# Optimization experiments

Measured on AMD Instinct MI355X. Metric: run time of the kernel, lower is better.

The kernel has to match this reference:

```python
import jax, jax.numpy as jnp
import numpy as np

N, E, IN, H, C = 50000, 400000, 128, 8, 32
NEG_SLOPE = 0.2


def setup_inputs() -> dict:
    key = jax.random.key(0)
    ks = jax.random.split(key, 8)
    s = 0.1
    return {
        "x": jax.random.normal(ks[0], (N, IN), jnp.float32),
        "edge_index": jax.random.randint(ks[1], (2, E), 0, N, dtype=jnp.int32),
        "edge_attr": jax.random.normal(ks[2], (E, 1), jnp.float32),
        "batch": jnp.zeros((N,), jnp.int32),
        "W_l": jax.random.normal(ks[3], (H * C, IN), jnp.float32) * s,
        "W_r": jax.random.normal(ks[4], (H * C, IN), jnp.float32) * s,
        "W_e": jax.random.normal(ks[5], (H * C, 1), jnp.float32) * s,
        "att": jax.random.normal(ks[6], (H, C), jnp.float32) * s,
        "bias": jnp.zeros((C,), jnp.float32),
        "W_proj": jax.random.normal(ks[7], (C, IN), jnp.float32) * s,
    }


def reference(x, edge_index, edge_attr, batch, W_l, W_r, W_e, att, bias, W_proj):
    n = x.shape[0]
    # --- add self loops (PyG default), edge_attr fill = 'mean' ---
    loop = jnp.arange(n, dtype=edge_index.dtype)
    ei = jnp.concatenate([edge_index, jnp.stack([loop, loop])], axis=1)  # [2, E+N]
    loop_attr = jnp.broadcast_to(edge_attr.mean(axis=0), (n, edge_attr.shape[1]))
    ea = jnp.concatenate([edge_attr, loop_attr], axis=0)                 # [E+N, 1]
    src, dst = ei[0], ei[1]

    # --- node transforms (GATv2: separate lin_l / lin_r) ---
    x_l = (x @ W_l.T).reshape(n, H, C)   # source-side features
    x_r = (x @ W_r.T).reshape(n, H, C)   # destination-side features
    e_feat = (ea @ W_e.T).reshape(-1, H, C)  # [E+N, H, C] edge fusion

    # --- GATv2 attention logits ---
    m = x_l[src] + x_r[dst] + e_feat                 # [E+N, H, C]
    m = jax.nn.leaky_relu(m, NEG_SLOPE)
    alpha = jnp.einsum("ehc,hc->eh", m, att)         # [E+N, H]

    # --- softmax over edges grouped by destination node ---
    amax = jax.ops.segment_max(alpha, dst, num_segments=n)  # [N, H]
    aexp = jnp.exp(alpha - amax[dst])
    denom = jax.ops.segment_sum(aexp, dst, num_segments=n)
    alpha = aexp / denom[dst]                        # [E+N, H]

    # --- weighted aggregation of source messages ---
    out = jax.ops.segment_sum(x_l[src] * alpha[:, :, None], dst, num_segments=n)  # [N, H, C]
    out = out.mean(axis=1) + bias                    # concat=False -> head mean, [N, C]

    # --- relu + projected residual ---
    x_new = jax.nn.relu(out) + x @ W_proj.T          # [N, C]
    return (x_new, alpha)
```

## Files before the change

### kernel.cpp

```cpp
#include <hip/hip_runtime.h>
#include <math.h>

#define N_NODES 50000
#define N_EDGES 400000
#define EN_TOT  450000
#define IN_DIM  128
#define H_HEADS 8
#define C_CH    32
#define HC      256
#define NEG_SLOPE 0.2f
#define MAXDEG 64

typedef __attribute__((ext_vector_type(8))) short bf16x8;
typedef __attribute__((ext_vector_type(4))) float f32x4;

#define OFF_XLB   0
#define OFF_XRB   (OFF_XLB + N_NODES * 128)
#define OFF_PROJ  (OFF_XRB + N_NODES * 128)
#define OFF_AEXP  (OFF_PROJ + N_NODES * C_CH)
#define OFF_WCAT  (OFF_AEXP + EN_TOT * H_HEADS)
#define OFF_PART  (OFF_WCAT + 34816)
#define OFF_MEAN  (OFF_PART + 1024)
#define OFF_PAD   (OFF_MEAN + 1)
#define OFF_CSR2  (OFF_PAD + 3)
#define OFF_DEG   (OFF_CSR2 + EN_TOT * 2)
#define OFF_OFFS  (OFF_DEG + N_NODES)
#define OFF_CUR   (OFF_OFFS + N_NODES + 1)
#define OFF_BSUM  (OFF_CUR + N_NODES)

#define SCAN_B 196
#define LOG2E 1.4426950408889634f

__device__ __forceinline__ unsigned f2bf(float f) {
    unsigned u = __float_as_uint(f);
    u += 0x7fffu + ((u >> 16) & 1u);
    return u >> 16;
}
__device__ __forceinline__ float bflo(unsigned u) { return __uint_as_float(u << 16); }
__device__ __forceinline__ float bfhi(unsigned u) { return __uint_as_float(u & 0xffff0000u); }

#define WCHUNKS 8704
__global__ __launch_bounds__(256) void pre_kernel(
    const float* __restrict__ Wl, const float* __restrict__ Wr, const float* __restrict__ Wproj,
    unsigned short* __restrict__ wcat,
    const int* __restrict__ ei, const float* __restrict__ ea,
    int* __restrict__ deg, float* __restrict__ part)
{
    __shared__ float sd[256];
    const int t = threadIdx.x;
    const int g = blockIdx.x * 256 + t;

    if (g < WCHUNKS) {
        int j = (g * 8) >> 7, k = (g * 8) & 127;
        const float* src = (j < 256 ? Wl + (size_t)j * 128
                                    : (j < 512 ? Wr + (size_t)(j - 256) * 128
                                               : Wproj + (size_t)(j - 512) * 128)) + k;
        float4 a = ((const float4*)src)[0];
        float4 b = ((const float4*)src)[1];
        uint4 o;
        o.x = f2bf(a.x) | (f2bf(a.y) << 16);
        o.y = f2bf(a.z) | (f2bf(a.w) << 16);
        o.z = f2bf(b.x) | (f2bf(b.y) << 16);
        o.w = f2bf(b.z) | (f2bf(b.w) << 16);
        ((uint4*)wcat)[g] = o;
    }

    float s = 0.f;
    for (int i = g; i < N_EDGES; i += 1024 * 256) s += ea[i];
    for (int i = g; i < EN_TOT; i += 1024 * 256) {
        int d = (i < N_EDGES) ? ei[N_EDGES + i] : (i - N_EDGES);
        atomicAdd(&deg[d], 1);
    }
    sd[t] = s; __syncthreads();
    for (int w = 128; w > 0; w >>= 1) { if (t < w) sd[t] += sd[t + w]; __syncthreads(); }
    if (t == 0) part[blockIdx.x] = sd[0];
}

__global__ __launch_bounds__(256) void scan_part_kernel(const int* __restrict__ deg,
                                                        int* __restrict__ bsum) {
    __shared__ int sd[256];
    int t = threadIdx.x;
    int i = blockIdx.x * 256 + t;
    int v = (i < N_NODES) ? deg[i] : 0;
    sd[t] = v; __syncthreads();
    for (int w = 128; w > 0; w >>= 1) { if (t < w) sd[t] += sd[t + w]; __syncthreads(); }
    if (t == 0) bsum[blockIdx.x] = sd[0];
}

__global__ __launch_bounds__(256) void mid_kernel(int* __restrict__ bsum,
                                                  const float* __restrict__ part,
                                                  float* __restrict__ mean_out) {
    __shared__ int sd[256];
    __shared__ float sf[256];
    int t = threadIdx.x;
    float s = part[t] + part[t + 256] + part[t + 512] + part[t + 768];
    sf[t] = s;
    int v = (t < SCAN_B) ? bsum[t] : 0;
    sd[t] = v; __syncthreads();
    for (int w = 128; w > 0; w >>= 1) { if (t < w) sf[t] += sf[t + w]; __syncthreads(); }
    if (t == 0) mean_out[0] = sf[0] / (float)N_EDGES;
    #pragma unroll
    for (int ofs = 1; ofs < 256; ofs <<= 1) {
        int u = (t >= ofs) ? sd[t - ofs] : 0;
        __syncthreads();
        sd[t] += u;
        __syncthreads();
    }
    if (t < SCAN_B) bsum[t] = sd[t] - v;
}

__global__ __launch_bounds__(256) void scan_final_kernel(
    const int* __restrict__ deg, const int* __restrict__ bsum,
    int* __restrict__ offs, int* __restrict__ cur) {
    __shared__ int sd[256];
    int t = threadIdx.x;
    int i = blockIdx.x * 256 + t;
    int v = (i < N_NODES) ? deg[i] : 0;
    sd[t] = v; __syncthreads();
    #pragma unroll
    for (int ofs = 1; ofs < 256; ofs <<= 1) {
        int u = (t >= ofs) ? sd[t - ofs] : 0;
        __syncthreads();
        sd[t] += u;
        __syncthreads();
    }
    int excl = bsum[blockIdx.x] + sd[t] - v;
    if (i < N_NODES) { offs[i] = excl; cur[i] = excl; }
    if (i == N_NODES - 1) offs[N_NODES] = excl + v;
}

__global__ __launch_bounds__(256) void scatter_kernel(
    const int* __restrict__ ei, const float* __restrict__ edge_attr,
    const float* __restrict__ mean_attr, int* __restrict__ cur,
    int2* __restrict__ csr2)
{
    int e = blockIdx.x * 256 + threadIdx.x;
    if (e >= EN_TOT) return;
    int s, d; float eav;
    if (e < N_EDGES) { s = ei[e]; d = ei[N_EDGES + e]; eav = edge_attr[e]; }
    else { s = e - N_EDGES; d = s; eav = mean_attr[0]; }
    int pos = atomicAdd(&cur[d], 1);
    csr2[pos] = make_int2(s | (int)(f2bf(eav) << 16), e);
}

#define GM 128
#define GN 64
#define CST 72

__global__ __launch_bounds__(256) void gemm_mfma_kernel(
    const float* __restrict__ x, const unsigned short* __restrict__ wcat,
    unsigned short* __restrict__ xlb, unsigned short* __restrict__ xrb,
    float* __restrict__ proj)
{
    __shared__ unsigned short As[GM * 128];
    __shared__ unsigned short Bs[GN * 128];
    const int t = threadIdx.x;
    const int m0 = blockIdx.x * GM;
    const int n0 = blockIdx.y * GN;

    #pragma unroll
    for (int cc = 0; cc < 8; ++cc) {
        int c = t + cc * 256;
        int r = c >> 4;
        int k0 = (c & 15) * 8;
        int row = m0 + r;
        uint4 o = make_uint4(0, 0, 0, 0);
        if (row < N_NODES) {
            const float* p = x + (size_t)row * IN_DIM + k0;
            float4 a = ((const float4*)p)[0];
            float4 b = ((const float4*)p)[1];
            o.x = f2bf(a.x) | (f2bf(a.y) << 16);
            o.y = f2bf(a.z) | (f2bf(a.w) << 16);
            o.z = f2bf(b.x) | (f2bf(b.y) << 16);
            o.w = f2bf(b.z) | (f2bf(b.w) << 16);
        }
        int byte = (r * 256 + k0 * 2) ^ ((r & 7) << 4);
        *((uint4*)((char*)As + byte)) = o;
    }
    #pragma unroll
    for (int cc = 0; cc < 4; ++cc) {
        int c = t + cc * 256;
        int r = c >> 4;
        int k0 = (c & 15) * 8;
        int j = n0 + r;
        uint4 v = make_uint4(0, 0, 0, 0);
        if (j < 544) v = *((const uint4*)(wcat + (size_t)j * 128 + k0));
        int byte = (r * 256 + k0 * 2) ^ ((r & 7) << 4);
        *((uint4*)((char*)Bs + byte)) = v;
    }
    __syncthreads();

    const int wid = t >> 6, lane = t & 63;
    const int wr = wid >> 1, wc = wid & 1;
    const int lrow = lane & 15;
    const int kgrp = (lane >> 4) * 8;

    f32x4 acc[4][2] = {};
    #pragma unroll
    for (int kk = 0; kk < 4; ++kk) {
        bf16x8 a[4], b[2];
        #pragma unroll
        for (int fm = 0; fm < 4; ++fm) {
            int r = wr * 64 + fm * 16 + lrow;
            int byte = (r * 256 + (kk * 32 + kgrp) * 2) ^ ((r & 7) << 4);
            a[fm] = *((const bf16x8*)((const char*)As + byte));
        }
        #pragma unroll
        for (int fn = 0; fn < 2; ++fn) {
            int r = wc * 32 + fn * 16 + lrow;
            int byte = (r * 256 + (kk * 32 + kgrp) * 2) ^ ((r & 7) << 4);
            b[fn] = *((const bf16x8*)((const char*)Bs + byte));
        }
        #pragma unroll
        for (int fm = 0; fm < 4; ++fm)
            #pragma unroll
            for (int fn = 0; fn < 2; ++fn)
                acc[fm][fn] = __builtin_amdgcn_mfma_f32_16x16x32_bf16(a[fm], b[fn], acc[fm][fn], 0, 0, 0);
    }

    const int crow0 = (lane >> 4) * 4;
    const int ccol = lane & 15;

    if (n0 < 512) {
        __syncthreads();
        unsigned short* Cs = As;
        #pragma unroll
        for (int fm = 0; fm < 4; ++fm)
            #pragma unroll
            for (int fn = 0; fn < 2; ++fn)
                #pragma unroll
                for (int r = 0; r < 4; ++r) {
                    int lr = wr * 64 + fm * 16 + crow0 + r;
                    int lc = wc * 32 + fn * 16 + ccol;
                    Cs[lr * CST + lc] = (unsigned short)f2bf(acc[fm][fn][r]);
                }
        __syncthreads();
        unsigned short* dst = (n0 < 256) ? xlb : xrb;
        const int colbase = n0 & 255;
        #pragma unroll
        for (int cc = 0; cc < 4; ++cc) {
            int c = t + cc * 256;
            int r = c >> 3;
            int c8 = (c & 7) * 8;
            int row = m0 + r;
            if (row < N_NODES) {
                uint4 v = *((const uint4*)(Cs + r * CST + c8));
                *((uint4*)(dst + (size_t)row * HC + colbase + c8)) = v;
            }
        }
    } else {
        #pragma unroll
        for (int fm = 0; fm < 4; ++fm)
            #pragma unroll
            for (int fn = 0; fn < 2; ++fn)
                #pragma unroll
                for (int r = 0; r < 4; ++r) {
                    int row = m0 + wr * 64 + fm * 16 + crow0 + r;
                    int col = n0 + wc * 32 + fn * 16 + ccol;
                    if (row >= N_NODES || col >= 544) continue;
                    proj[(size_t)row * C_CH + (col - 512)] = acc[fm][fn][r];
                }
    }
}

__global__ __launch_bounds__(256) void node_agg_kernel(
    const int* __restrict__ offs, const int2* __restrict__ csr2,
    const float* __restrict__ We, const float* __restrict__ att,
    const unsigned short* __restrict__ xlb, const unsigned short* __restrict__ xrb,
    const float* __restrict__ proj, const float* __restrict__ bias,
    float* __restrict__ aexp_ovf, float* __restrict__ alpha_out, float* __restrict__ xnew)
{
    __shared__ float s_aexp[4][MAXDEG][H_HEADS];
    __shared__ int   s_eid[4][MAXDEG];
    const int w = threadIdx.x >> 6;
    const int l = threadIdx.x & 63;
    const int d = blockIdx.x * 4 + w;
    if (d >= N_NODES) return;
    const int half = l >> 5;
    const int sl = l & 31;

    const float4 we0 = ((const float4*)We)[sl * 2];
    const float4 we1 = ((const float4*)We)[sl * 2 + 1];
    const float4 at0 = ((const float4*)att)[sl * 2];
    const float4 at1 = ((const float4*)att)[sl * 2 + 1];
    const float wev[8] = {we0.x, we0.y, we0.z, we0.w, we1.x, we1.y, we1.z, we1.w};
    const float atv[8] = {at0.x * LOG2E, at0.y * LOG2E, at0.z * LOG2E, at0.w * LOG2E,
                          at1.x * LOG2E, at1.y * LOG2E, at1.z * LOG2E, at1.w * LOG2E};

    const uint4 vru = ((const uint4*)(xrb + (size_t)d * HC))[sl];
    float vr[8];
    vr[0] = bflo(vru.x); vr[1] = bfhi(vru.x); vr[2] = bflo(vru.y); vr[3] = bfhi(vru.y);
    vr[4] = bflo(vru.z); vr[5] = bfhi(vru.z); vr[6] = bflo(vru.w); vr[7] = bfhi(vru.w);

    const int beg = offs[d];
    const int end = offs[d + 1];

    float acc[8] = {0.f, 0.f, 0.f, 0.f, 0.f, 0.f, 0.f, 0.f};
    float den = 0.f;

    int i = beg;
    int2 c0 = make_int2(0, 0);
    uint4 vl0 = make_uint4(0, 0, 0, 0);
    if (i + half < end) {
        c0 = csr2[i + half];
        vl0 = ((const uint4*)(xlb + (size_t)(c0.x & 0xffff) * HC))[sl];
    }
    while (i < end) {
        const int ni = i + 2;
        int2 c1 = make_int2(0, 0);
        uint4 vl1 = make_uint4(0, 0, 0, 0);
        if (ni + half < end) {
            c1 = csr2[ni + half];
            vl1 = ((const uint4*)(xlb + (size_t)(c1.x & 0xffff) * HC))[sl];
        }

        const float ea = bfhi((unsigned)c0.x);
        float xv[8];
        xv[0] = bflo(vl0.x); xv[1] = bfhi(vl0.x); xv[2] = bflo(vl0.y); xv[3] = bfhi(vl0.y);
        xv[4] = bflo(vl0.z); xv[5] = bfhi(vl0.z); xv[6] = bflo(vl0.w); xv[7] = bfhi(vl0.w);

        float tt = 0.f;
        #pragma unroll
        for (int j = 0; j < 8; ++j) {
            float m = xv[j] + vr[j] + ea * wev[j];
            m = fmaxf(m, NEG_SLOPE * m);
            tt += m * atv[j];
        }
        tt += __shfl_xor(tt, 1);
        tt += __shfl_xor(tt, 2);
        float aex = exp2f(tt);
        const bool valid = (i + half) < end;
        aex = valid ? aex : 0.f;
        const int li = i + half - beg;
        if (valid && (sl & 3) == 0) {
            if (li < MAXDEG) s_aexp[w][li][sl >> 2] = aex;
            else             aexp_ovf[(size_t)c0.y * H_HEADS + (sl >> 2)] = aex;
        }
        if (valid && sl == 0 && li < MAXDEG) s_eid[w][li] = c0.y;
        #pragma unroll
        for (int j = 0; j < 8; ++j) acc[j] += aex * xv[j];
        den += aex;

        c0 = c1; vl0 = vl1; i = ni;
    }

    den += __shfl_xor(den, 32);
    #pragma unroll
    for (int j = 0; j < 8; ++j) acc[j] += __shfl_xor(acc[j], 32);

    const float den_h = __shfl(den, ((l & 7) << 2));
    const float rden = 1.f / den_h;
    for (int b = beg; b < end; b += 8) {
        const int idx = b + (l >> 3);
        if (idx < end) {
            const int li = idx - beg;
            int e; float ax;
            if (li < MAXDEG) { e = s_eid[w][li]; ax = s_aexp[w][li][l & 7]; }
            else { e = csr2[idx].y; ax = aexp_ovf[(size_t)e * H_HEADS + (l & 7)]; }
            alpha_out[(size_t)e * H_HEADS + (l & 7)] = ax * rden;
        }
    }

    const float inv = 1.f / den;
    #pragma unroll
    for (int j = 0; j < 8; ++j) acc[j] *= inv;
    #pragma unroll
    for (int mask = 4; mask <= 16; mask <<= 1)
        #pragma unroll
        for (int j = 0; j < 8; ++j) acc[j] += __shfl_xor(acc[j], mask);
    if (half == 0 && sl < 4) {
        const float4 bi0 = ((const float4*)bias)[sl * 2];
        const float4 bi1 = ((const float4*)bias)[sl * 2 + 1];
        const float4 pr0 = ((const float4*)(proj + (size_t)d * C_CH))[sl * 2];
        const float4 pr1 = ((const float4*)(proj + (size_t)d * C_CH))[sl * 2 + 1];
        float4 r0, r1;
        r0.x = fmaxf(acc[0] * 0.125f + bi0.x, 0.f) + pr0.x;
        r0.y = fmaxf(acc[1] * 0.125f + bi0.y, 0.f) + pr0.y;
        r0.z = fmaxf(acc[2] * 0.125f + bi0.z, 0.f) + pr0.z;
        r0.w = fmaxf(acc[3] * 0.125f + bi0.w, 0.f) + pr0.w;
        r1.x = fmaxf(acc[4] * 0.125f + bi1.x, 0.f) + pr1.x;
        r1.y = fmaxf(acc[5] * 0.125f + bi1.y, 0.f) + pr1.y;
        r1.z = fmaxf(acc[6] * 0.125f + bi1.z, 0.f) + pr1.z;
        r1.w = fmaxf(acc[7] * 0.125f + bi1.w, 0.f) + pr1.w;
        ((float4*)(xnew + (size_t)d * C_CH))[sl * 2] = r0;
        ((float4*)(xnew + (size_t)d * C_CH))[sl * 2 + 1] = r1;
    }
}

extern "C" void kernel_launch(void* const* d_in, const int* in_sizes, int n_in,
                              void* d_out, int out_size, void* d_ws, size_t ws_size,
                              hipStream_t stream) {
    const float* x         = (const float*)d_in[0];
    const int*   ei        = (const int*)d_in[1];
    const float* edge_attr = (const float*)d_in[2];
    const float* Wl        = (const float*)d_in[4];
    const float* Wr        = (const float*)d_in[5];
    const float* We        = (const float*)d_in[6];
    const float* att       = (const float*)d_in[7];
    const float* bias      = (const float*)d_in[8];
    const float* Wproj     = (const float*)d_in[9];

    float* ws    = (float*)d_ws;
    unsigned short* xlb  = (unsigned short*)(ws + OFF_XLB);
    unsigned short* xrb  = (unsigned short*)(ws + OFF_XRB);
    float* proj  = ws + OFF_PROJ;
    float* aexp  = ws + OFF_AEXP;
    unsigned short* wcat = (unsigned short*)(ws + OFF_WCAT);
    float* part  = ws + OFF_PART;
    float* meanp = ws + OFF_MEAN;
    int2*  csr2  = (int2*)(ws + OFF_CSR2);
    int*   deg   = (int*)(ws + OFF_DEG);
    int*   offs  = (int*)(ws + OFF_OFFS);
    int*   cur   = (int*)(ws + OFF_CUR);
    int*   bsum  = (int*)(ws + OFF_BSUM);

    float* out_xnew  = (float*)d_out;
    float* out_alpha = (float*)d_out + (size_t)N_NODES * C_CH;

    hipMemsetAsync(deg, 0, N_NODES * sizeof(int), stream);

    pre_kernel<<<1024, 256, 0, stream>>>(Wl, Wr, Wproj, wcat, ei, edge_attr, deg, part);

    scan_part_kernel<<<SCAN_B, 256, 0, stream>>>(deg, bsum);
    mid_kernel<<<1, 256, 0, stream>>>(bsum, part, meanp);
    scan_final_kernel<<<SCAN_B, 256, 0, stream>>>(deg, bsum, offs, cur);

    scatter_kernel<<<(EN_TOT + 255) / 256, 256, 0, stream>>>(ei, edge_attr, meanp, cur, csr2);

    dim3 ggrid((N_NODES + GM - 1) / GM, (544 + GN - 1) / GN);
    gemm_mfma_kernel<<<ggrid, 256, 0, stream>>>(x, wcat, xlb, xrb, proj);

    node_agg_kernel<<<(N_NODES + 3) / 4, 256, 0, stream>>>(offs, csr2, We, att, xlb, xrb,
                                                           proj, bias, aexp, out_alpha, out_xnew);
}
```

Before: 173.0 us.

## Fuse CSR scan and scatter kernels into one cooperative kernel with grid syncs

Replaces the four small kernels that build the CSR (block-sum, middle scan plus mean, final scan, edge scatter) with a single cooperative launch of 784 blocks that separates the phases with grid.sync. This removes three kernel launches and their gaps between dependent stages. The cost is three grid-wide barriers, and the scatter now runs as a grid-stride loop over fewer blocks. The cooperative launch also requires all 784 blocks to be resident at once.

```diff
diff --git a/kernel.cpp b/kernel.cpp
--- a/kernel.cpp
+++ b/kernel.cpp
@@ -1,4 +1,5 @@
 #include <hip/hip_runtime.h>
+#include <hip/hip_cooperative_groups.h>
 #include <math.h>
 
 #define N_NODES 50000
@@ -29,6 +30,7 @@
 #define OFF_BSUM  (OFF_CUR + N_NODES)
 
 #define SCAN_B 196
+#define CSRB   784
 #define LOG2E 1.4426950408889634f
 
 __device__ __forceinline__ unsigned f2bf(float f) {
@@ -76,71 +78,73 @@
     if (t == 0) part[blockIdx.x] = sd[0];
 }
 
-__global__ __launch_bounds__(256) void scan_part_kernel(const int* __restrict__ deg,
-                                                        int* __restrict__ bsum) {
-    __shared__ int sd[256];
-    int t = threadIdx.x;
-    int i = blockIdx.x * 256 + t;
-    int v = (i < N_NODES) ? deg[i] : 0;
-    sd[t] = v; __syncthreads();
-    for (int w = 128; w > 0; w >>= 1) { if (t < w) sd[t] += sd[t + w]; __syncthreads(); }
-    if (t == 0) bsum[blockIdx.x] = sd[0];
-}
-
-__global__ __launch_bounds__(256) void mid_kernel(int* __restrict__ bsum,
-                                                  const float* __restrict__ part,
-                                                  float* __restrict__ mean_out) {
+__global__ __launch_bounds__(256) void csr_build_kernel(
+    const int* __restrict__ ei, const float* __restrict__ ea,
+    const float* __restrict__ part,
+    int* __restrict__ deg, int* __restrict__ bsum,
+    int* __restrict__ offs, int* __restrict__ cur,
+    float* __restrict__ mean_out, int2* __restrict__ csr2)
+{
+    namespace cg = cooperative_groups;
+    cg::grid_group grid = cg::this_grid();
     __shared__ int sd[256];
     __shared__ float sf[256];
-    int t = threadIdx.x;
-    float s = part[t] + part[t + 256] + part[t + 512] + part[t + 768];
-    sf[t] = s;
-    int v = (t < SCAN_B) ? bsum[t] : 0;
-    sd[t] = v; __syncthreads();
-    for (int w = 128; w > 0; w >>= 1) { if (t < w) sf[t] += sf[t + w]; __syncthreads(); }
-    if (t == 0) mean_out[0] = sf[0] / (float)N_EDGES;
-    #pragma unroll
-    for (int ofs = 1; ofs < 256; ofs <<= 1) {
-        int u = (t >= ofs) ? sd[t - ofs] : 0;
-        __syncthreads();
-        sd[t] += u;
-        __syncthreads();
-    }
-    if (t < SCAN_B) bsum[t] = sd[t] - v;
-}
-
-__global__ __launch_bounds__(256) void scan_final_kernel(
-    const int* __restrict__ deg, const int* __restrict__ bsum,
-    int* __restrict__ offs, int* __restrict__ cur) {
-    __shared__ int sd[256];
-    int t = threadIdx.x;
-    int i = blockIdx.x * 256 + t;
-    int v = (i < N_NODES) ? deg[i] : 0;
-    sd[t] = v; __syncthreads();
-    #pragma unroll
-    for (int ofs = 1; ofs < 256; ofs <<= 1) {
-        int u = (t >= ofs) ? sd[t - ofs] : 0;
-        __syncthreads();
-        sd[t] += u;
-        __syncthreads();
-    }
-    int excl = bsum[blockIdx.x] + sd[t] - v;
-    if (i < N_NODES) { offs[i] = excl; cur[i] = excl; }
-    if (i == N_NODES - 1) offs[N_NODES] = excl + v;
-}
-
-__global__ __launch_bounds__(256) void scatter_kernel(
-    const int* __restrict__ ei, const float* __restrict__ edge_attr,
-    const float* __restrict__ mean_attr, int* __restrict__ cur,
-    int2* __restrict__ csr2)
-{
-    int e = blockIdx.x * 256 + threadIdx.x;
-    if (e >= EN_TOT) return;
-    int s, d; float eav;
-    if (e < N_EDGES) { s = ei[e]; d = ei[N_EDGES + e]; eav = edge_attr[e]; }
-    else { s = e - N_EDGES; d = s; eav = mean_attr[0]; }
-    int pos = atomicAdd(&cur[d], 1);
-    csr2[pos] = make_int2(s | (int)(f2bf(eav) << 16), e);
+    const int t = threadIdx.x;
+    const int b = blockIdx.x;
+
+    if (b < SCAN_B) {
+        int i = b * 256 + t;
+        int v = (i < N_NODES) ? deg[i] : 0;
+        sd[t] = v; __syncthreads();
+        for (int w = 128; w > 0; w >>= 1) { if (t < w) sd[t] += sd[t + w]; __syncthreads(); }
+        if (t == 0) bsum[b] = sd[0];
+    }
+    grid.sync();
+
+    if (b == 0) {
+        float s = part[t] + part[t + 256] + part[t + 512] + part[t + 768];
+        sf[t] = s;
+        int v = (t < SCAN_B) ? bsum[t] : 0;
+        sd[t] = v; __syncthreads();
+        for (int w = 128; w > 0; w >>= 1) { if (t < w) sf[t] += sf[t + w]; __syncthreads(); }
+        if (t == 0) mean_out[0] = sf[0] / (float)N_EDGES;
+        #pragma unroll
+        for (int ofs = 1; ofs < 256; ofs <<= 1) {
+            int u = (t >= ofs) ? sd[t - ofs] : 0;
+            __syncthreads();
+            sd[t] += u;
+            __syncthreads();
+        }
+        if (t < SCAN_B) bsum[t] = sd[t] - v;
+    }
+    grid.sync();
+
+    if (b < SCAN_B) {
+        int i = b * 256 + t;
+        int v = (i < N_NODES) ? deg[i] : 0;
+        sd[t] = v; __syncthreads();
+        #pragma unroll
+        for (int ofs = 1; ofs < 256; ofs <<= 1) {
+            int u = (t >= ofs) ? sd[t - ofs] : 0;
+            __syncthreads();
+            sd[t] += u;
+            __syncthreads();
+        }
+        int excl = bsum[b] + sd[t] - v;
+        if (i < N_NODES) { offs[i] = excl; cur[i] = excl; }
+        if (i == N_NODES - 1) offs[N_NODES] = excl + v;
+    }
+    grid.sync();
+
+    const float mv = mean_out[0];
+    const int stride = CSRB * 256;
+    for (int e = b * 256 + t; e < EN_TOT; e += stride) {
+        int s, d; float eav;
+        if (e < N_EDGES) { s = ei[e]; d = ei[N_EDGES + e]; eav = ea[e]; }
+        else { s = e - N_EDGES; d = s; eav = mv; }
+        int pos = atomicAdd(&cur[d], 1);
+        csr2[pos] = make_int2(s | (int)(f2bf(eav) << 16), e);
+    }
 }
 
 #define GM 128
@@ -421,11 +425,13 @@
 
     pre_kernel<<<1024, 256, 0, stream>>>(Wl, Wr, Wproj, wcat, ei, edge_attr, deg, part);
 
-    scan_part_kernel<<<SCAN_B, 256, 0, stream>>>(deg, bsum);
-    mid_kernel<<<1, 256, 0, stream>>>(bsum, part, meanp);
-    scan_final_kernel<<<SCAN_B, 256, 0, stream>>>(deg, bsum, offs, cur);
-
-    scatter_kernel<<<(EN_TOT + 255) / 256, 256, 0, stream>>>(ei, edge_attr, meanp, cur, csr2);
+    {
+        void* args[] = {(void*)&ei, (void*)&edge_attr, (void*)&part,
+                        (void*)&deg, (void*)&bsum, (void*)&offs, (void*)&cur,
+                        (void*)&meanp, (void*)&csr2};
+        hipLaunchCooperativeKernel((const void*)csr_build_kernel,
+                                   dim3(CSRB), dim3(256), args, 0, stream);
+    }
 
     dim3 ggrid((N_NODES + GM - 1) / GM, (544 + GN - 1) / GN);
     gemm_mfma_kernel<<<ggrid, 256, 0, stream>>>(x, wcat, xlb, xrb, proj);
```

Result: slower. 437.3 us (+152.8%).
